# Optimization experiments

Measured on AMD Instinct MI355X. Metric: run time of the kernel, lower is better.

Reference implementation:

```python
import jax, jax.numpy as jnp
import numpy as np

B, C, HW = 128, 3, 224
P = 16
D = 256
NH = 8
HD = D // NH
E = 4            # num_experts
K = 2            # top-k
FF = 4 * D
NC = 38
EPS = 1e-5


def _layernorm(x, g, b):
    mu = jnp.mean(x, axis=-1, keepdims=True)
    var = jnp.mean(jnp.square(x - mu), axis=-1, keepdims=True)
    return (x - mu) * jax.lax.rsqrt(var + EPS) * g + b


def setup_inputs() -> dict:
    key = jax.random.key(0)
    ks = jax.random.split(key, 16)
    s = 0.02
    return {
        "x": jax.random.normal(ks[0], (B, C, HW, HW), dtype=jnp.float32),
        "conv_w": jax.random.normal(ks[1], (D, C, P, P), dtype=jnp.float32) * s,
        "conv_b": jnp.zeros((D,), jnp.float32),
        "cls_token": jnp.zeros((1, 1, D), jnp.float32),
        "ln1_g": jnp.ones((D,), jnp.float32),
        "ln1_b": jnp.zeros((D,), jnp.float32),
        "qkv_w": jax.random.normal(ks[2], (3 * D, D), dtype=jnp.float32) * s,
        "qkv_b": jnp.zeros((3 * D,), jnp.float32),
        "out_w": jax.random.normal(ks[3], (D, D), dtype=jnp.float32) * s,
        "out_b": jnp.zeros((D,), jnp.float32),
        "ln2_g": jnp.ones((D,), jnp.float32),
        "ln2_b": jnp.zeros((D,), jnp.float32),
        "router_w": jax.random.normal(ks[4], (E, D), dtype=jnp.float32) * s,
        "router_b": jnp.zeros((E,), jnp.float32),
        "e_w1": jax.random.normal(ks[5], (E, D, FF), dtype=jnp.float32) * s,
        "e_b1": jnp.zeros((E, FF), jnp.float32),
        "e_w2": jax.random.normal(ks[6], (E, FF, D), dtype=jnp.float32) * s,
        "e_b2": jnp.zeros((E, D), jnp.float32),
        "head_w": jax.random.normal(ks[7], (NC, D), dtype=jnp.float32) * s,
        "head_b": jnp.zeros((NC,), jnp.float32),
    }


def reference(x, conv_w, conv_b, cls_token, ln1_g, ln1_b, qkv_w, qkv_b,
              out_w, out_b, ln2_g, ln2_b, router_w, router_b,
              e_w1, e_b1, e_w2, e_b2, head_w, head_b):
    # patch embed: Conv2d(3, D, 16, 16) -> [B, D, 14, 14] -> [B, 196, D]
    h = jax.lax.conv_general_dilated(
        x, conv_w, window_strides=(P, P), padding="VALID",
        dimension_numbers=("NCHW", "OIHW", "NCHW")) + conv_b[None, :, None, None]
    b = h.shape[0]
    tok = h.reshape(b, D, -1).transpose(0, 2, 1)            # [B, 196, D]
    tok = jnp.concatenate([jnp.broadcast_to(cls_token, (b, 1, D)), tok], axis=1)  # [B, 197, D]
    S = tok.shape[1]

    # Multi-head self-attention (pre-norm)
    x2 = _layernorm(tok, ln1_g, ln1_b)
    qkv = x2 @ qkv_w.T + qkv_b                              # [B, S, 3D]
    q, k, v = jnp.split(qkv, 3, axis=-1)
    q = q.reshape(b, S, NH, HD)
    k = k.reshape(b, S, NH, HD)
    v = v.reshape(b, S, NH, HD)
    scores = jnp.einsum("bqhd,bkhd->bhqk", q, k) / np.float32(np.sqrt(HD))
    attn = jax.nn.softmax(scores, axis=-1)
    ao = jnp.einsum("bhqk,bkhd->bqhd", attn, v).reshape(b, S, D)
    ao = ao @ out_w.T + out_b
    tok = tok + ao

    # MoE FFN (pre-norm). NOTE: original code computes top-k routing weights
    # but never multiplies outputs by them — outputs of selected experts are
    # simply summed. We reproduce that faithfully.
    x2 = _layernorm(tok, ln2_g, ln2_b)
    x_flat = x2.reshape(-1, D)                              # [T, D]
    logits = x_flat @ router_w.T + router_b                 # [T, E]
    probs = jax.nn.softmax(logits, axis=-1)
    _topw, topi = jax.lax.top_k(probs, K)                   # topw unused (as in source)
    mask = (topi[..., None] == jnp.arange(E)).any(axis=1)   # [T, E] bool
    out_flat = jnp.zeros_like(x_flat)
    for i in range(E):                                       # fixed small expert count
        hid = jax.nn.gelu(x_flat @ e_w1[i] + e_b1[i], approximate=False)
        out_flat = out_flat + mask[:, i:i + 1].astype(x_flat.dtype) * (hid @ e_w2[i] + e_b2[i])
    tok = tok + out_flat.reshape(b, S, D)

    return tok[:, 0] @ head_w.T + head_b                    # [B, NC]
```

## Files before the change

### kernel.cpp

```cpp
#include <hip/hip_runtime.h>
#include <hip/hip_bf16.h>
#include <math.h>

#define TTOK   25216
#define SEQL   197
#define NBATCH 128
#define DMODEL 256
#define NHEADS 8
#define FFD    1024
#define NEXP   4
#define NCLS   38
#define CONVK  768
#define NPATCH 196
#define CM     25088

typedef unsigned short u16;
typedef unsigned int u32;
using s16x4 = __attribute__((ext_vector_type(4))) short;
using s16x8 = __attribute__((ext_vector_type(8))) short;
using f32x4 = __attribute__((ext_vector_type(4))) float;

__device__ __forceinline__ float b2f(u16 v) {
  union { unsigned u; float f; } x; x.u = (unsigned)v << 16; return x.f;
}
__device__ __forceinline__ u16 f2b(float f) {
  __hip_bfloat16 h = __float2bfloat16(f);
  return *reinterpret_cast<u16*>(&h);
}
__device__ __forceinline__ void gload16(const void* g, void* l) {
  __builtin_amdgcn_global_load_lds(
      (const __attribute__((address_space(1))) void*)g,
      (__attribute__((address_space(3))) void*)l, 16, 0, 0);
}
__device__ __forceinline__ float warp_sum(float v) {
  #pragma unroll
  for (int o = 32; o; o >>= 1) v += __shfl_xor(v, o);
  return v;
}
__device__ __forceinline__ float warp_max(float v) {
  #pragma unroll
  for (int o = 32; o; o >>= 1) v = fmaxf(v, __shfl_xor(v, o));
  return v;
}
__device__ __forceinline__ int fsw(int row) { return (row ^ (row >> 2)) & 3; }
__device__ __forceinline__ s16x8 ldA72(const u16* base, int rowa, int l4) {
  const char* p = (const char*)base + rowa * 72 + l4 * 16;
  s16x4 a = *(const s16x4*)p;
  s16x4 b = *(const s16x4*)(p + 8);
  return __builtin_shufflevector(a, b, 0, 1, 2, 3, 4, 5, 6, 7);
}

__global__ __launch_bounds__(256) void k_cast2(const float* __restrict__ in,
                                               u16* __restrict__ hi,
                                               u16* __restrict__ lo) {
  int i = (blockIdx.x * 256 + threadIdx.x) * 4;
  float4 v = *(const float4*)&in[i];
  float vv[4] = {v.x, v.y, v.z, v.w};
  u16 h[4], l[4];
  #pragma unroll
  for (int j = 0; j < 4; ++j) {
    h[j] = f2b(vv[j]);
    l[j] = f2b(vv[j] - b2f(h[j]));
  }
  *(uint2*)&hi[i] = *(const uint2*)h;
  *(uint2*)&lo[i] = *(const uint2*)l;
}

__global__ __launch_bounds__(256) void k_conv(const float* __restrict__ x,
                                              const u16* __restrict__ cwh,
                                              const u16* __restrict__ cwl,
                                              const float* __restrict__ cb,
                                              float* __restrict__ tok) {
  const int n0 = blockIdx.x * 128;
  const int m0 = blockIdx.y * 128;
  __shared__ __align__(16) u16 lds[25600];
  u16* Ah_s = lds;
  u16* Al_s = lds + 4608;
  u16* Wbuf = lds + 9216;
  const int tid = threadIdx.x;
  const int lane = tid & 63;
  const int wv = tid >> 6;
  const int wr = wv >> 1, wc = wv & 1;
  const int l15 = lane & 15, l4 = lane >> 4;
  f32x4 acc[4][4] = {};

  const int kpos = (tid & 7) * 4;
  long abase[4]; int aldso[4];
  #pragma unroll
  for (int it = 0; it < 4; ++it) {
    int row = it * 32 + (tid >> 3);
    int m = m0 + row;
    int b = m / NPATCH, p = m - b * NPATCH;
    int py = p / 14, px = p - py * 14;
    abase[it] = (long)(b * 3) * 50176 + (py * 16) * 224 + px * 16;
    aldso[it] = row * 72 + kpos * 2;
  }
  long woff[2]; int wofs[2];
  #pragma unroll
  for (int r = 0; r < 2; ++r) {
    int off = r * 4096 + tid * 16;
    int row = off >> 6;
    int c16 = (off >> 4) & 3;
    int kk = (c16 ^ fsw(row)) << 3;
    woff[r] = (long)(n0 + row) * CONVK + kk;
    wofs[r] = off;
  }
  #pragma unroll
  for (int r = 0; r < 2; ++r) {
    gload16(cwh + woff[r], (char*)Wbuf + wofs[r]);
    gload16(cwl + woff[r], (char*)Wbuf + 8192 + wofs[r]);
  }
  float4 xr[4];
  {
    int c = kpos >> 8, r8 = kpos & 255;
    long soff = (long)c * 50176 + (r8 >> 4) * 224 + (r8 & 15);
    #pragma unroll
    for (int it = 0; it < 4; ++it) xr[it] = *(const float4*)&x[abase[it] + soff];
  }
  int cur = 0;
  for (int kc = 0; kc < CONVK; kc += 32) {
    #pragma unroll
    for (int it = 0; it < 4; ++it) {
      float vv[4] = {xr[it].x, xr[it].y, xr[it].z, xr[it].w};
      u16 h[4], l[4];
      #pragma unroll
      for (int j = 0; j < 4; ++j) {
        h[j] = f2b(vv[j]);
        l[j] = f2b(vv[j] - b2f(h[j]));
      }
      *(uint2*)((char*)Ah_s + aldso[it]) = *(const uint2*)h;
      *(uint2*)((char*)Al_s + aldso[it]) = *(const uint2*)l;
    }
    __syncthreads();
    if (kc + 32 < CONVK) {
      char* wdst = (char*)Wbuf + ((cur ^ 1) << 14);
      #pragma unroll
      for (int r = 0; r < 2; ++r) {
        gload16(cwh + woff[r] + kc + 32, wdst + wofs[r]);
        gload16(cwl + woff[r] + kc + 32, wdst + 8192 + wofs[r]);
      }
      int k = kc + 32 + kpos;
      int c = k >> 8, r8 = k & 255;
      long soff = (long)c * 50176 + (r8 >> 4) * 224 + (r8 & 15);
      #pragma unroll
      for (int it = 0; it < 4; ++it) xr[it] = *(const float4*)&x[abase[it] + soff];
    }
    const char* Wcur = (const char*)Wbuf + (cur << 14);
    s16x8 ah[4], al[4], bh[4], bl[4];
    #pragma unroll
    for (int i = 0; i < 4; ++i) {
      int rowa = wr * 64 + i * 16 + l15;
      ah[i] = ldA72(Ah_s, rowa, l4);
      al[i] = ldA72(Al_s, rowa, l4);
      int rowb = wc * 64 + i * 16 + l15;
      int kbb = (l4 ^ fsw(rowb)) << 4;
      bh[i] = *(const s16x8*)(Wcur + rowb * 64 + kbb);
      bl[i] = *(const s16x8*)(Wcur + 8192 + rowb * 64 + kbb);
    }
    #pragma unroll
    for (int i = 0; i < 4; ++i)
      #pragma unroll
      for (int j = 0; j < 4; ++j)
        acc[i][j] = __builtin_amdgcn_mfma_f32_16x16x32_bf16(ah[i], bh[j],
                                                            acc[i][j], 0, 0, 0);
    #pragma unroll
    for (int i = 0; i < 4; ++i)
      #pragma unroll
      for (int j = 0; j < 4; ++j)
        acc[i][j] = __builtin_amdgcn_mfma_f32_16x16x32_bf16(ah[i], bl[j],
                                                            acc[i][j], 0, 0, 0);
    #pragma unroll
    for (int i = 0; i < 4; ++i)
      #pragma unroll
      for (int j = 0; j < 4; ++j)
        acc[i][j] = __builtin_amdgcn_mfma_f32_16x16x32_bf16(al[i], bh[j],
                                                            acc[i][j], 0, 0, 0);
    __syncthreads();
    cur ^= 1;
  }
  const int mb = m0 + wr * 64 + (l4 << 2);
  const int nb = n0 + wc * 64 + l15;
  #pragma unroll
  for (int i = 0; i < 4; ++i) {
    #pragma unroll
    for (int jf = 0; jf < 4; ++jf) {
      #pragma unroll
      for (int j = 0; j < 4; ++j) {
        int m = mb + i * 16 + j;
        int n = nb + jf * 16;
        int bq = m / NPATCH;
        long cr = (long)bq * SEQL + (m - bq * NPATCH) + 1;
        tok[cr * DMODEL + n] = acc[i][jf][j] + cb[n];
      }
    }
  }
}

__global__ __launch_bounds__(256) void k_lnstat(const float* __restrict__ in,
                                                float2* __restrict__ st) {
  const int row = blockIdx.x * 4 + (threadIdx.x >> 6);
  const int lane = threadIdx.x & 63;
  float4 v = *(const float4*)&in[(size_t)row * DMODEL + lane * 4];
  float s1 = v.x + v.y + v.z + v.w;
  float s2 = v.x * v.x + v.y * v.y + v.z * v.z + v.w * v.w;
  s1 = warp_sum(s1);
  s2 = warp_sum(s2);
  if (lane == 0) {
    float mu = s1 * (1.f / DMODEL);
    float var = s2 * (1.f / DMODEL) - mu * mu;
    st[row] = make_float2(mu, rsqrtf(var + 1e-5f));
  }
}

__global__ __launch_bounds__(256) void k_qkv(const float* __restrict__ tok,
                                             const float2* __restrict__ stats,
                                             const float* __restrict__ g,
                                             const float* __restrict__ bb,
                                             const u16* __restrict__ Wh,
                                             const u16* __restrict__ Wl,
                                             const float* __restrict__ bias,
                                             float* __restrict__ Cf) {
  const int n0 = blockIdx.x * 128;
  const int m0 = blockIdx.y * 128;
  __shared__ __align__(16) u16 lds[25600];
  u16* Ah_s = lds;
  u16* Al_s = lds + 4608;
  u16* Wbuf = lds + 9216;
  const int tid = threadIdx.x;
  const int lane = tid & 63;
  const int wv = tid >> 6;
  const int wr = wv >> 1, wc = wv & 1;
  const int l15 = lane & 15, l4 = lane >> 4;
  f32x4 acc[4][4] = {};

  const int kpos = (tid & 7) * 4;
  long atok[4]; float2 st[4]; int aldso[4];
  #pragma unroll
  for (int it = 0; it < 4; ++it) {
    int row = it * 32 + (tid >> 3);
    int m = m0 + row;
    atok[it] = (long)m * DMODEL;
    st[it] = stats[m];
    aldso[it] = row * 72 + kpos * 2;
  }
  long woff[2]; int wofs[2];
  #pragma unroll
  for (int r = 0; r < 2; ++r) {
    int off = r * 4096 + tid * 16;
    int row = off >> 6;
    int c16 = (off >> 4) & 3;
    int kk = (c16 ^ fsw(row)) << 3;
    woff[r] = (long)(n0 + row) * DMODEL + kk;
    wofs[r] = off;
  }
  #pragma unroll
  for (int r = 0; r < 2; ++r) {
    gload16(Wh + woff[r], (char*)Wbuf + wofs[r]);
    gload16(Wl + woff[r], (char*)Wbuf + 8192 + wofs[r]);
  }
  float4 xr[4], gr, br;
  #pragma unroll
  for (int it = 0; it < 4; ++it) xr[it] = *(const float4*)&tok[atok[it] + kpos];
  gr = *(const float4*)&g[kpos];
  br = *(const float4*)&bb[kpos];
  int cur = 0;
  for (int kc = 0; kc < DMODEL; kc += 32) {
    float gg[4] = {gr.x, gr.y, gr.z, gr.w};
    float bbv[4] = {br.x, br.y, br.z, br.w};
    #pragma unroll
    for (int it = 0; it < 4; ++it) {
      float vv[4] = {xr[it].x, xr[it].y, xr[it].z, xr[it].w};
      u16 h[4], l[4];
      #pragma unroll
      for (int j = 0; j < 4; ++j) {
        float xd = (vv[j] - st[it].x) * st[it].y * gg[j] + bbv[j];
        h[j] = f2b(xd);
        l[j] = f2b(xd - b2f(h[j]));
      }
      *(uint2*)((char*)Ah_s + aldso[it]) = *(const uint2*)h;
      *(uint2*)((char*)Al_s + aldso[it]) = *(const uint2*)l;
    }
    __syncthreads();
    if (kc + 32 < DMODEL) {
      char* wdst = (char*)Wbuf + ((cur ^ 1) << 14);
      #pragma unroll
      for (int r = 0; r < 2; ++r) {
        gload16(Wh + woff[r] + kc + 32, wdst + wofs[r]);
        gload16(Wl + woff[r] + kc + 32, wdst + 8192 + wofs[r]);
      }
      #pragma unroll
      for (int it = 0; it < 4; ++it)
        xr[it] = *(const float4*)&tok[atok[it] + kc + 32 + kpos];
      gr = *(const float4*)&g[kc + 32 + kpos];
      br = *(const float4*)&bb[kc + 32 + kpos];
    }
    const char* Wcur = (const char*)Wbuf + (cur << 14);
    s16x8 ah[4], al[4], bh[4], bl[4];
    #pragma unroll
    for (int i = 0; i < 4; ++i) {
      int rowa = wr * 64 + i * 16 + l15;
      ah[i] = ldA72(Ah_s, rowa, l4);
      al[i] = ldA72(Al_s, rowa, l4);
      int rowb = wc * 64 + i * 16 + l15;
      int kbb = (l4 ^ fsw(rowb)) << 4;
      bh[i] = *(const s16x8*)(Wcur + rowb * 64 + kbb);
      bl[i] = *(const s16x8*)(Wcur + 8192 + rowb * 64 + kbb);
    }
    #pragma unroll
    for (int i = 0; i < 4; ++i)
      #pragma unroll
      for (int j = 0; j < 4; ++j)
        acc[i][j] = __builtin_amdgcn_mfma_f32_16x16x32_bf16(ah[i], bh[j],
                                                            acc[i][j], 0, 0, 0);
    #pragma unroll
    for (int i = 0; i < 4; ++i)
      #pragma unroll
      for (int j = 0; j < 4; ++j)
        acc[i][j] = __builtin_amdgcn_mfma_f32_16x16x32_bf16(ah[i], bl[j],
                                                            acc[i][j], 0, 0, 0);
    #pragma unroll
    for (int i = 0; i < 4; ++i)
      #pragma unroll
      for (int j = 0; j < 4; ++j)
        acc[i][j] = __builtin_amdgcn_mfma_f32_16x16x32_bf16(al[i], bh[j],
                                                            acc[i][j], 0, 0, 0);
    __syncthreads();
    cur ^= 1;
  }
  const int mb = m0 + wr * 64 + (l4 << 2);
  const int nb = n0 + wc * 64 + l15;
  #pragma unroll
  for (int i = 0; i < 4; ++i) {
    #pragma unroll
    for (int jf = 0; jf < 4; ++jf) {
      #pragma unroll
      for (int j = 0; j < 4; ++j) {
        int m = mb + i * 16 + j;
        int n = nb + jf * 16;
        Cf[(long)m * 512 + n] = acc[i][jf][j] + bias[n];
      }
    }
  }
}

__global__ void k_cls(const float* __restrict__ cls, float* __restrict__ tok) {
  tok[(size_t)blockIdx.x * SEQL * DMODEL + threadIdx.x] = cls[threadIdx.x];
}

__global__ __launch_bounds__(256) void k_qcls(const float* __restrict__ tok,
                                              const float2* __restrict__ stats,
                                              const float* __restrict__ g,
                                              const float* __restrict__ bb,
                                              const u16* __restrict__ qwh,
                                              const u16* __restrict__ qwl,
                                              const float* __restrict__ qb,
                                              u16* __restrict__ qch,
                                              u16* __restrict__ qcl) {
  const int b = blockIdx.x, n = threadIdx.x;
  __shared__ float xs[DMODEL];
  float2 st = stats[b * SEQL];
  float v = tok[(size_t)b * SEQL * DMODEL + n];
  xs[n] = (v - st.x) * st.y * g[n] + bb[n];
  __syncthreads();
  float val = qb[n];
  #pragma unroll 4
  for (int i = 0; i < 32; ++i) {
    s16x8 wh = *(const s16x8*)(qwh + (size_t)n * DMODEL + i * 8);
    s16x8 wl = *(const s16x8*)(qwl + (size_t)n * DMODEL + i * 8);
    #pragma unroll
    for (int j = 0; j < 8; ++j)
      val = fmaf(b2f((u16)wh[j]) + b2f((u16)wl[j]), xs[i * 8 + j], val);
  }
  u16 h = f2b(val);
  qch[b * DMODEL + n] = h;
  qcl[b * DMODEL + n] = f2b(val - b2f(h));
}

__global__ __launch_bounds__(256) void k_attn_cls(const u16* __restrict__ qch,
                                                  const u16* __restrict__ qcl,
                                                  const float* __restrict__ kvf,
                                                  float* __restrict__ ao) {
  const int w = threadIdx.x >> 6, lane = threadIdx.x & 63;
  const int unit = blockIdx.x * 4 + w;
  const int b = unit >> 3, h = unit & 7;
  __shared__ float Ss[4][200];
  float q[32];
  #pragma unroll
  for (int i = 0; i < 4; ++i) {
    s16x8 vh = *(const s16x8*)(qch + b * DMODEL + h * 32 + i * 8);
    s16x8 vl = *(const s16x8*)(qcl + b * DMODEL + h * 32 + i * 8);
    #pragma unroll
    for (int j = 0; j < 8; ++j) q[i * 8 + j] = b2f((u16)vh[j]) + b2f((u16)vl[j]);
  }
  float sc[4];
  float mx = -1e30f;
  #pragma unroll
  for (int r = 0; r < 4; ++r) {
    int k = lane + 64 * r;
    float s = -1e30f;
    if (k < SEQL) {
      const float* kr = kvf + ((size_t)(b * SEQL + k)) * 512 + h * 32;
      s = 0.f;
      #pragma unroll
      for (int i = 0; i < 8; ++i) {
        float4 kv4 = *(const float4*)(kr + i * 4);
        s = fmaf(kv4.x, q[i * 4 + 0], s);
        s = fmaf(kv4.y, q[i * 4 + 1], s);
        s = fmaf(kv4.z, q[i * 4 + 2], s);
        s = fmaf(kv4.w, q[i * 4 + 3], s);
      }
      s *= 0.17677669529663687f;
    }
    sc[r] = s;
    mx = fmaxf(mx, s);
  }
  mx = warp_max(mx);
  float sm = 0.f;
  #pragma unroll
  for (int r = 0; r < 4; ++r) {
    int k = lane + 64 * r;
    float e = (k < SEQL) ? __expf(sc[r] - mx) : 0.f;
    sc[r] = e;
    sm += e;
  }
  sm = warp_sum(sm);
  float inv = 1.f / sm;
  #pragma unroll
  for (int r = 0; r < 4; ++r) {
    int k = lane + 64 * r;
    if (k < SEQL) Ss[w][k] = sc[r] * inv;
  }
  int d = lane & 31, half = lane >> 5;
  float acc = 0.f;
  for (int i = 0; i < 99; ++i) {
    int k = half * 99 + i;
    if (k < SEQL)
      acc = fmaf(Ss[w][k], kvf[((size_t)(b * SEQL + k)) * 512 + 256 + h * 32 + d], acc);
  }
  acc += __shfl_xor(acc, 32);
  if (lane < 32) ao[(b * NHEADS + h) * 32 + d] = acc;
}

__global__ __launch_bounds__(256) void k_oproj_route(
    const float* __restrict__ ao, const float* __restrict__ ow,
    const float* __restrict__ ob, const float* __restrict__ tok,
    const float* __restrict__ g, const float* __restrict__ bb,
    const float* __restrict__ rw, const float* __restrict__ rb,
    float* __restrict__ tokc, float* __restrict__ x2cf,
    float* __restrict__ maskf) {
  const int b = blockIdx.x, n = threadIdx.x;
  const int w = n >> 6, lane = n & 63;
  __shared__ float xs[DMODEL];
  __shared__ float xd_s[DMODEL];
  __shared__ float red[8];
  __shared__ float lg[4];
  xs[n] = ao[b * DMODEL + n];
  __syncthreads();
  float val = ob[n];
  #pragma unroll 4
  for (int i = 0; i < 64; ++i) {
    float4 wv = *(const float4*)(ow + (size_t)n * DMODEL + i * 4);
    val = fmaf(wv.x, xs[i * 4 + 0], val);
    val = fmaf(wv.y, xs[i * 4 + 1], val);
    val = fmaf(wv.z, xs[i * 4 + 2], val);
    val = fmaf(wv.w, xs[i * 4 + 3], val);
  }
  float t = tok[(size_t)b * SEQL * DMODEL + n] + val;
  tokc[b * DMODEL + n] = t;
  float s1 = warp_sum(t), s2 = warp_sum(t * t);
  if (lane == 0) { red[w] = s1; red[4 + w] = s2; }
  __syncthreads();
  s1 = red[0] + red[1] + red[2] + red[3];
  s2 = red[4] + red[5] + red[6] + red[7];
  float mu = s1 * (1.f / DMODEL);
  float var = s2 * (1.f / DMODEL) - mu * mu;
  float rs = rsqrtf(var + 1e-5f);
  float xd = (t - mu) * rs * g[n] + bb[n];
  x2cf[b * DMODEL + n] = xd;
  xd_s[n] = xd;
  __syncthreads();
  float s = 0.f;
  #pragma unroll
  for (int i = 0; i < 4; ++i) s = fmaf(xd_s[lane + i * 64], rw[w * DMODEL + lane + i * 64], s);
  s = warp_sum(s) + rb[w];
  if (lane == 0) lg[w] = s;
  __syncthreads();
  if (n < NEXP) {
    int e = n;
    int rank = 0;
    #pragma unroll
    for (int j = 0; j < NEXP; ++j)
      if (j != e && (lg[j] > lg[e] || (lg[j] == lg[e] && j < e))) ++rank;
    maskf[b * NEXP + e] = (rank < 2) ? 1.f : 0.f;
  }
}

__global__ __launch_bounds__(256) void k_moe1(const float* __restrict__ x2cf,
                                              const float* __restrict__ w1,
                                              const float* __restrict__ b1,
                                              const float* __restrict__ maskf,
                                              float* __restrict__ hid) {
  const int e = blockIdx.x, t = blockIdx.y;
  if (maskf[t * NEXP + e] == 0.f) return;
  __shared__ float xs[DMODEL];
  const int tid = threadIdx.x;
  xs[tid] = x2cf[t * DMODEL + tid];
  __syncthreads();
  const float* w1e = w1 + (size_t)e * DMODEL * FFD + tid;
  float a0 = 0.f, a1 = 0.f, a2 = 0.f, a3 = 0.f;
  #pragma unroll 4
  for (int k = 0; k < DMODEL; ++k) {
    float xv = xs[k];
    const float* wr_ = w1e + (size_t)k * FFD;
    a0 = fmaf(xv, wr_[0], a0);
    a1 = fmaf(xv, wr_[256], a1);
    a2 = fmaf(xv, wr_[512], a2);
    a3 = fmaf(xv, wr_[768], a3);
  }
  float accs[4] = {a0, a1, a2, a3};
  float* hrow = hid + ((size_t)e * NBATCH + t) * FFD;
  #pragma unroll
  for (int j = 0; j < 4; ++j) {
    float v = accs[j] + b1[e * FFD + tid + j * 256];
    hrow[tid + j * 256] = 0.5f * v * (1.0f + erff(v * 0.70710678118654752f));
  }
}

__global__ __launch_bounds__(256) void k_moe2(const float* __restrict__ hid,
                                              const float* __restrict__ w2,
                                              const float* __restrict__ b2,
                                              const float* __restrict__ maskf,
                                              float* __restrict__ tokc) {
  const int t = blockIdx.x, dc = blockIdx.y;
  const int tid = threadIdx.x;
  const int dl = tid & 127, kh = tid >> 7;
  const int dout = dc * 128 + dl;
  int e0 = 0;
  while (e0 < 3 && maskf[t * NEXP + e0] == 0.f) ++e0;
  int e1 = e0 + 1;
  while (e1 < 3 && maskf[t * NEXP + e1] == 0.f) ++e1;
  __shared__ float hs0[FFD], hs1[FFD];
  const float* h0 = hid + ((size_t)e0 * NBATCH + t) * FFD;
  const float* h1 = hid + ((size_t)e1 * NBATCH + t) * FFD;
  for (int i = tid * 4; i < FFD; i += 1024) {
    *(float4*)&hs0[i] = *(const float4*)&h0[i];
    *(float4*)&hs1[i] = *(const float4*)&h1[i];
  }
  __syncthreads();
  const float* w20 = w2 + (size_t)e0 * FFD * DMODEL + dout;
  const float* w21 = w2 + (size_t)e1 * FFD * DMODEL + dout;
  float a0 = 0.f, a1 = 0.f;
  const int k0 = kh * 512;
  #pragma unroll 8
  for (int k = k0; k < k0 + 512; ++k) {
    a0 = fmaf(hs0[k], w20[(size_t)k * DMODEL], a0);
    a1 = fmaf(hs1[k], w21[(size_t)k * DMODEL], a1);
  }
  __shared__ float red[256];
  red[tid] = a0 + a1;
  __syncthreads();
  if (kh == 0) {
    float full = red[dl] + red[128 + dl] +
                 b2[e0 * DMODEL + dout] + b2[e1 * DMODEL + dout];
    tokc[t * DMODEL + dout] += full;
  }
}

__global__ __launch_bounds__(256) void k_head(const float* __restrict__ tokc,
                                              const float* __restrict__ hw,
                                              const float* __restrict__ hb,
                                              float* __restrict__ out) {
  int b = blockIdx.x;
  int w = threadIdx.x >> 6, lane = threadIdx.x & 63;
  const float* row = tokc + (size_t)b * DMODEL;
  for (int c = w; c < NCLS; c += 4) {
    float s = 0.f;
    for (int d = lane; d < DMODEL; d += 64) s = fmaf(row[d], hw[c * DMODEL + d], s);
    s = warp_sum(s);
    if (lane == 0) out[b * NCLS + c] = s + hb[c];
  }
}

extern "C" void kernel_launch(void* const* d_in, const int* in_sizes, int n_in,
                              void* d_out, int out_size, void* d_ws, size_t ws_size,
                              hipStream_t stream) {
  const float* x      = (const float*)d_in[0];
  const float* conv_w = (const float*)d_in[1];
  const float* conv_b = (const float*)d_in[2];
  const float* cls    = (const float*)d_in[3];
  const float* ln1g   = (const float*)d_in[4];
  const float* ln1b   = (const float*)d_in[5];
  const float* qkv_w  = (const float*)d_in[6];
  const float* qkv_b  = (const float*)d_in[7];
  const float* out_w  = (const float*)d_in[8];
  const float* out_b  = (const float*)d_in[9];
  const float* ln2g   = (const float*)d_in[10];
  const float* ln2b   = (const float*)d_in[11];
  const float* rw     = (const float*)d_in[12];
  const float* rb     = (const float*)d_in[13];
  const float* e_w1   = (const float*)d_in[14];
  const float* e_b1   = (const float*)d_in[15];
  const float* e_w2   = (const float*)d_in[16];
  const float* e_b2   = (const float*)d_in[17];
  const float* head_w = (const float*)d_in[18];
  const float* head_b = (const float*)d_in[19];
  float* out = (float*)d_out;

  char* ws = (char*)d_ws;
  size_t off = 0;
  auto alloc = [&](size_t bytes) {
    void* p = ws + off;
    off += (bytes + 255) & ~(size_t)255;
    return p;
  };
  float*  tok   = (float*)alloc((size_t)TTOK * DMODEL * 4);
  float*  qkvf  = (float*)alloc((size_t)TTOK * 512 * 4);
  float2* stats = (float2*)alloc((size_t)TTOK * 8);
  u16*    cwh   = (u16*)alloc((size_t)DMODEL * CONVK * 2);
  u16*    cwl   = (u16*)alloc((size_t)DMODEL * CONVK * 2);
  u16*    qwh   = (u16*)alloc((size_t)768 * DMODEL * 2);
  u16*    qwl   = (u16*)alloc((size_t)768 * DMODEL * 2);
  u16*    qch   = (u16*)alloc((size_t)NBATCH * DMODEL * 2);
  u16*    qcl   = (u16*)alloc((size_t)NBATCH * DMODEL * 2);
  float*  aocf  = (float*)alloc((size_t)NBATCH * DMODEL * 4);
  float*  tokc  = (float*)alloc((size_t)NBATCH * DMODEL * 4);
  float*  x2cf  = (float*)alloc((size_t)NBATCH * DMODEL * 4);
  float*  maskf = (float*)alloc((size_t)NBATCH * NEXP * 4);
  float*  hid   = (float*)alloc((size_t)NEXP * NBATCH * FFD * 4);

  k_cast2<<<192, 256, 0, stream>>>(conv_w, cwh, cwl);
  k_cast2<<<192, 256, 0, stream>>>(qkv_w, qwh, qwl);

  k_conv<<<dim3(2, CM / 128), 256, 0, stream>>>(x, cwh, cwl, conv_b, tok);
  k_cls<<<NBATCH, DMODEL, 0, stream>>>(cls, tok);

  k_lnstat<<<TTOK / 4, 256, 0, stream>>>(tok, stats);

  k_qkv<<<dim3(4, TTOK / 128), 256, 0, stream>>>(
      tok, stats, ln1g, ln1b, qwh + 256 * DMODEL, qwl + 256 * DMODEL,
      qkv_b + 256, qkvf);

  k_qcls<<<NBATCH, 256, 0, stream>>>(tok, stats, ln1g, ln1b, qwh, qwl, qkv_b,
                                     qch, qcl);

  k_attn_cls<<<NBATCH * NHEADS / 4, 256, 0, stream>>>(qch, qcl, qkvf, aocf);

  k_oproj_route<<<NBATCH, 256, 0, stream>>>(aocf, out_w, out_b, tok,
                                            ln2g, ln2b, rw, rb,
                                            tokc, x2cf, maskf);

  k_moe1<<<dim3(NEXP, NBATCH), 256, 0, stream>>>(x2cf, e_w1, e_b1, maskf, hid);
  k_moe2<<<dim3(NBATCH, 2), 256, 0, stream>>>(hid, e_w2, e_b2, maskf, tokc);

  k_head<<<NBATCH, 256, 0, stream>>>(tokc, head_w, head_b, out);
}
```

Baseline: 211.3 us.

## Split-K patch-embed conv, fuse bias/cls/LN-stats finish, merge weight casts

```diff
diff --git a/kernel.cpp b/kernel.cpp
--- a/kernel.cpp
+++ b/kernel.cpp
@@ -13,6 +13,7 @@
 #define CONVK  768
 #define NPATCH 196
 #define CM     25088
+#define KSPL   384
 
 typedef unsigned short u16;
 typedef unsigned int u32;
@@ -50,10 +51,16 @@
   return __builtin_shufflevector(a, b, 0, 1, 2, 3, 4, 5, 6, 7);
 }
 
-__global__ __launch_bounds__(256) void k_cast2(const float* __restrict__ in,
-                                               u16* __restrict__ hi,
-                                               u16* __restrict__ lo) {
-  int i = (blockIdx.x * 256 + threadIdx.x) * 4;
+__global__ __launch_bounds__(256) void k_cast2b(const float* __restrict__ cw,
+                                                u16* __restrict__ cwh,
+                                                u16* __restrict__ cwl,
+                                                const float* __restrict__ qw,
+                                                u16* __restrict__ qwh,
+                                                u16* __restrict__ qwl) {
+  int bid = blockIdx.x;
+  const float* in = cw; u16* hi = cwh; u16* lo = cwl;
+  if (bid >= 192) { bid -= 192; in = qw; hi = qwh; lo = qwl; }
+  int i = (bid * 256 + threadIdx.x) * 4;
   float4 v = *(const float4*)&in[i];
   float vv[4] = {v.x, v.y, v.z, v.w};
   u16 h[4], l[4];
@@ -69,10 +76,10 @@
 __global__ __launch_bounds__(256) void k_conv(const float* __restrict__ x,
                                               const u16* __restrict__ cwh,
                                               const u16* __restrict__ cwl,
-                                              const float* __restrict__ cb,
-                                              float* __restrict__ tok) {
+                                              float* __restrict__ part) {
   const int n0 = blockIdx.x * 128;
   const int m0 = blockIdx.y * 128;
+  const int kbase = blockIdx.z * KSPL;
   __shared__ __align__(16) u16 lds[25600];
   u16* Ah_s = lds;
   u16* Al_s = lds + 4608;
@@ -102,7 +109,7 @@
     int row = off >> 6;
     int c16 = (off >> 4) & 3;
     int kk = (c16 ^ fsw(row)) << 3;
-    woff[r] = (long)(n0 + row) * CONVK + kk;
+    woff[r] = (long)(n0 + row) * CONVK + kbase + kk;
     wofs[r] = off;
   }
   #pragma unroll
@@ -112,13 +119,14 @@
   }
   float4 xr[4];
   {
-    int c = kpos >> 8, r8 = kpos & 255;
+    int k = kbase + kpos;
+    int c = k >> 8, r8 = k & 255;
     long soff = (long)c * 50176 + (r8 >> 4) * 224 + (r8 & 15);
     #pragma unroll
     for (int it = 0; it < 4; ++it) xr[it] = *(const float4*)&x[abase[it] + soff];
   }
   int cur = 0;
-  for (int kc = 0; kc < CONVK; kc += 32) {
+  for (int kc = 0; kc < KSPL; kc += 32) {
     #pragma unroll
     for (int it = 0; it < 4; ++it) {
       float vv[4] = {xr[it].x, xr[it].y, xr[it].z, xr[it].w};
@@ -132,14 +140,14 @@
       *(uint2*)((char*)Al_s + aldso[it]) = *(const uint2*)l;
     }
     __syncthreads();
-    if (kc + 32 < CONVK) {
+    if (kc + 32 < KSPL) {
       char* wdst = (char*)Wbuf + ((cur ^ 1) << 14);
       #pragma unroll
       for (int r = 0; r < 2; ++r) {
         gload16(cwh + woff[r] + kc + 32, wdst + wofs[r]);
         gload16(cwl + woff[r] + kc + 32, wdst + 8192 + wofs[r]);
       }
-      int k = kc + 32 + kpos;
+      int k = kbase + kc + 32 + kpos;
       int c = k >> 8, r8 = k & 255;
       long soff = (long)c * 50176 + (r8 >> 4) * 224 + (r8 & 15);
       #pragma unroll
@@ -178,6 +186,7 @@
     __syncthreads();
     cur ^= 1;
   }
+  float* pout = part + (size_t)blockIdx.z * CM * DMODEL;
   const int mb = m0 + wr * 64 + (l4 << 2);
   const int nb = n0 + wc * 64 + l15;
   #pragma unroll
@@ -188,21 +197,37 @@
       for (int j = 0; j < 4; ++j) {
         int m = mb + i * 16 + j;
         int n = nb + jf * 16;
-        int bq = m / NPATCH;
-        long cr = (long)bq * SEQL + (m - bq * NPATCH) + 1;
-        tok[cr * DMODEL + n] = acc[i][jf][j] + cb[n];
+        pout[(long)m * DMODEL + n] = acc[i][jf][j];
       }
     }
   }
 }
 
-__global__ __launch_bounds__(256) void k_lnstat(const float* __restrict__ in,
+__global__ __launch_bounds__(256) void k_finish(const float* __restrict__ p0,
+                                                const float* __restrict__ p1,
+                                                const float* __restrict__ cb,
+                                                const float* __restrict__ cls,
+                                                float* __restrict__ tok,
                                                 float2* __restrict__ st) {
   const int row = blockIdx.x * 4 + (threadIdx.x >> 6);
   const int lane = threadIdx.x & 63;
-  float4 v = *(const float4*)&in[(size_t)row * DMODEL + lane * 4];
-  float s1 = v.x + v.y + v.z + v.w;
-  float s2 = v.x * v.x + v.y * v.y + v.z * v.z + v.w * v.w;
+  const int b = row / SEQL, s = row - b * SEQL;
+  float vv[4];
+  if (s == 0) {
+    *(float4*)vv = *(const float4*)&cls[lane * 4];
+  } else {
+    long m = (long)b * NPATCH + s - 1;
+    float4 a = *(const float4*)&p0[m * DMODEL + lane * 4];
+    float4 c = *(const float4*)&p1[m * DMODEL + lane * 4];
+    float4 bi = *(const float4*)&cb[lane * 4];
+    vv[0] = a.x + c.x + bi.x;
+    vv[1] = a.y + c.y + bi.y;
+    vv[2] = a.z + c.z + bi.z;
+    vv[3] = a.w + c.w + bi.w;
+  }
+  *(float4*)&tok[(size_t)row * DMODEL + lane * 4] = *(const float4*)vv;
+  float s1 = vv[0] + vv[1] + vv[2] + vv[3];
+  float s2 = vv[0]*vv[0] + vv[1]*vv[1] + vv[2]*vv[2] + vv[3]*vv[3];
   s1 = warp_sum(s1);
   s2 = warp_sum(s2);
   if (lane == 0) {
@@ -341,10 +366,6 @@
       }
     }
   }
-}
-
-__global__ void k_cls(const float* __restrict__ cls, float* __restrict__ tok) {
-  tok[(size_t)blockIdx.x * SEQL * DMODEL + threadIdx.x] = cls[threadIdx.x];
 }
 
 __global__ __launch_bounds__(256) void k_qcls(const float* __restrict__ tok,
@@ -627,14 +648,14 @@
   float*  x2cf  = (float*)alloc((size_t)NBATCH * DMODEL * 4);
   float*  maskf = (float*)alloc((size_t)NBATCH * NEXP * 4);
   float*  hid   = (float*)alloc((size_t)NEXP * NBATCH * FFD * 4);
-
-  k_cast2<<<192, 256, 0, stream>>>(conv_w, cwh, cwl);
-  k_cast2<<<192, 256, 0, stream>>>(qkv_w, qwh, qwl);
-
-  k_conv<<<dim3(2, CM / 128), 256, 0, stream>>>(x, cwh, cwl, conv_b, tok);
-  k_cls<<<NBATCH, DMODEL, 0, stream>>>(cls, tok);
-
-  k_lnstat<<<TTOK / 4, 256, 0, stream>>>(tok, stats);
+  float* part = qkvf;
+
+  k_cast2b<<<384, 256, 0, stream>>>(conv_w, cwh, cwl, qkv_w, qwh, qwl);
+
+  k_conv<<<dim3(2, CM / 128, 2), 256, 0, stream>>>(x, cwh, cwl, part);
+
+  k_finish<<<TTOK / 4, 256, 0, stream>>>(part, part + (size_t)CM * DMODEL,
+                                         conv_b, cls, tok, stats);
 
   k_qkv<<<dim3(4, TTOK / 128), 256, 0, stream>>>(
       tok, stats, ln1g, ln1b, qwh + 256 * DMODEL, qwl + 256 * DMODEL,
```

Result: no change. 214.7 us (+1.6%).
